# Kernel tuning notes

Hardware: AMD Instinct MI355X
Metric: run time of the kernel (lower is better)

The kernel has to match this reference:

```python
import jax, jax.numpy as jnp
import numpy as np

N = 128   # image_size == proj_size
C = 16    # channels
B = 1
NUM_AP = 1
AP_ANGLES = np.linspace(0.0, 0.0, NUM_AP).tolist()
APLT_ANGLES = np.linspace(0.0, np.pi / 2, 2).tolist()
EPS = 1e-5


def _conv3d(x, w, b):
    # x: [B,C,D,H,W], w: [O,I,3,3,3]
    y = jax.lax.conv_general_dilated(
        x, w, window_strides=(1, 1, 1), padding='SAME',
        dimension_numbers=('NCDHW', 'OIDHW', 'NCDHW'))
    return y + b[None, :, None, None, None]


def _instance_norm(x):
    # InstanceNorm3d, affine=False: normalize per (batch, channel) over D,H,W
    m = x.mean(axis=(2, 3, 4), keepdims=True)
    v = x.var(axis=(2, 3, 4), keepdims=True)
    return (x - m) * jax.lax.rsqrt(v + EPS)


def _resblock(x, w1, b1, w2, b2):
    out = jax.nn.relu(_instance_norm(_conv3d(x, w1, b1)))
    out = _instance_norm(_conv3d(out, w2, b2)) + x
    return jax.nn.relu(out)


def _backproject(proj):
    # proj: [B,C,A,Z,U] -> volume [B,C,Z,N,N] (parallel-beam smear-back)
    c = (N - 1) / 2.0
    ys, xs = jnp.meshgrid(jnp.arange(N, dtype=jnp.float32),
                          jnp.arange(N, dtype=jnp.float32), indexing='ij')
    vol = jnp.zeros((proj.shape[0], proj.shape[1], proj.shape[3], N, N), proj.dtype)
    for a, th in enumerate(AP_ANGLES):
        u = np.cos(th) * (ys - c) + np.sin(th) * (xs - c) + c  # [N,N] detector coord
        u0 = jnp.clip(jnp.floor(u).astype(jnp.int32), 0, N - 2)
        w = u - u0.astype(u.dtype)
        p = proj[:, :, a]                     # [B,C,Z,U]
        g = p[..., u0] * (1.0 - w) + p[..., u0 + 1] * w   # [B,C,Z,N,N]
        valid = (u >= 0.0) & (u <= N - 1.0)
        vol = vol + jnp.where(valid, g, 0.0)
    return vol / float(len(AP_ANGLES))


def _forward_project(vol):
    # vol: [B,C,Z,H,W] -> proj [B,C,A,Z,U] (line integrals per z-slice)
    c = (N - 1) / 2.0
    uu, tt = jnp.meshgrid(jnp.arange(N, dtype=jnp.float32),
                          jnp.arange(N, dtype=jnp.float32), indexing='ij')
    projs = []
    for th in APLT_ANGLES:
        y = c + (uu - c) * np.cos(th) - (tt - c) * np.sin(th)
        x = c + (uu - c) * np.sin(th) + (tt - c) * np.cos(th)
        y0 = jnp.clip(jnp.floor(y).astype(jnp.int32), 0, N - 2)
        x0 = jnp.clip(jnp.floor(x).astype(jnp.int32), 0, N - 2)
        wy = y - y0.astype(y.dtype)
        wx = x - x0.astype(x.dtype)
        g = (vol[:, :, :, y0, x0] * (1 - wy) * (1 - wx)
             + vol[:, :, :, y0 + 1, x0] * wy * (1 - wx)
             + vol[:, :, :, y0, x0 + 1] * (1 - wy) * wx
             + vol[:, :, :, y0 + 1, x0 + 1] * wy * wx)   # [B,C,Z,U,T]
        valid = (y >= 0.0) & (y <= N - 1.0) & (x >= 0.0) & (x <= N - 1.0)
        projs.append(jnp.where(valid, g, 0.0).sum(axis=-1))  # sum over ray param t
    return jnp.stack(projs, axis=2)  # [B,C,A,Z,U]


def setup_inputs() -> dict:
    key = jax.random.key(0)
    ks = jax.random.split(key, 9)
    scale = 1.0 / np.sqrt(C * 27)
    inp = {'projection_data': jax.random.normal(ks[0], (B, C, NUM_AP, N, N), jnp.float32)}
    for i, name in enumerate(['a1', 'a2', 'b1', 'b2']):
        inp['w_' + name] = jax.random.normal(ks[1 + 2 * i], (C, C, 3, 3, 3), jnp.float32) * scale
        inp['b_' + name] = jax.random.normal(ks[2 + 2 * i], (C,), jnp.float32) * 0.01
    return inp


def reference(projection_data, w_a1, b_a1, w_a2, b_a2, w_b1, b_b1, w_b2, b_b2):
    vol = _backproject(projection_data)
    vol = _resblock(vol, w_a1, b_a1, w_a2, b_a2)
    vol = _resblock(vol, w_b1, b_b1, w_b2, b_b2)
    return _forward_project(vol)
```

## Files before the change

### kernel.cpp

```cpp
#include <hip/hip_runtime.h>


typedef unsigned short u16;
typedef unsigned int   u32;
using s16x8 = __attribute__((ext_vector_type(8))) short;
using f32x4 = __attribute__((ext_vector_type(4))) float;

#define IN_ELEMS 262144
#define MN_ELEMS 4194304
#define WS_NEED  28505408ull

__device__ __forceinline__ float bf2f(u16 h) {
    union { u32 u; float f; } v; v.u = ((u32)h) << 16; return v.f;
}
__device__ __forceinline__ u16 f2bf(float f) {
    union { float f; u32 u; } v; v.f = f;
    u32 u = v.u;
    return (u16)((u + 0x7fffu + ((u >> 16) & 1u)) >> 16);
}
__device__ __forceinline__ float ldin(const void* p, int i, int bf) {
    return bf ? bf2f(((const u16*)p)[i]) : ((const float*)p)[i];
}
__device__ __forceinline__ u16 ldbf(const void* p, int i, int bf) {
    return bf ? ((const u16*)p)[i] : f2bf(((const float*)p)[i]);
}
__device__ __forceinline__ void unpack8(uint4 a, float* f) {
    u32 w[4] = {a.x, a.y, a.z, a.w};
#pragma unroll
    for (int i = 0; i < 4; i++) {
        f[2*i]   = bf2f((u16)(w[i] & 0xffff));
        f[2*i+1] = bf2f((u16)(w[i] >> 16));
    }
}
__device__ __forceinline__ void unpack4(uint2 a, float* f) {
    f[0] = bf2f((u16)(a.x & 0xffff)); f[1] = bf2f((u16)(a.x >> 16));
    f[2] = bf2f((u16)(a.y & 0xffff)); f[3] = bf2f((u16)(a.y >> 16));
}

__global__ void sentinel_k(u16* __restrict__ out, int n)
{
    int i = blockIdx.x * 256 + threadIdx.x;
    if (i < n) out[i] = 0x4640;
}

__global__ __launch_bounds__(256) void wprep_prep_k(
    const void* __restrict__ w0, const void* __restrict__ w1,
    const void* __restrict__ w2, const void* __restrict__ w3,
    const void* __restrict__ b0, const void* __restrict__ b1,
    const void* __restrict__ b2, const void* __restrict__ b3,
    const void* __restrict__ proj,
    float* __restrict__ st, int* __restrict__ flag,
    float* __restrict__ biasf, float* __restrict__ w2d,
    float* __restrict__ pz, u16* __restrict__ afrag,
    float* __restrict__ I0, u16* __restrict__ M0)
{
    const int tid = threadIdx.x;
    const u16* pp = (const u16*)w0;
    int cnt = 0;
    for (int i = 0; i < 32; i++) {
        int e = (pp[2 * i] >> 7) & 0xFF;
        if (e >= 64 && e <= 130) cnt++;
    }
    const int bf = (cnt >= 24) ? 1 : 0;
    const void* WS[4] = {w0, w1, w2, w3};
    const void* BS[4] = {b0, b1, b2, b3};
    const int b = blockIdx.x;

    if (b >= 135) {
        const int bb = b - 135;
        const int d = bb >> 2;
        const int ys = (bb & 3) * 32;
        for (int i = tid; i < 512; i += 256) {
            int y = ys + (i >> 4), c = i & 15;
            I0[(d * 128 + y) * 16 + c] = ldin(proj, c * 16384 + d * 128 + y, bf);
        }
        for (int i = tid; i < 1024; i += 256) {
            int y = ys + (i >> 5), x = (i >> 1) & 15, hh = i & 1;
            bool on = (x <= 4) | (x == 7) | (x >= 8 && x < 12);
            u32 pw[4] = {0u, 0u, 0u, 0u};
            if (on) {
#pragma unroll
                for (int j = 0; j < 4; j++) {
                    int c0 = hh * 8 + 2 * j;
                    u16 a = f2bf(ldin(proj, c0 * 16384 + d * 128 + y, bf));
                    u16 bb2 = f2bf(ldin(proj, (c0 + 1) * 16384 + d * 128 + y, bf));
                    pw[j] = (u32)a | ((u32)bb2 << 16);
                }
            }
            *(uint4*)(M0 + ((d * 128 + y) << 8) + (x << 4) + hh * 8) =
                make_uint4(pw[0], pw[1], pw[2], pw[3]);
        }
        return;
    }

    if (b < 18) {
        int gi = b * 256 + tid;
        int L = gi / 1152, r = gi - L * 1152;
        int fi = r >> 6, l = r & 63;
        int kzky = fi >> 1, grp = fi & 1;
        int kz = kzky / 3, ky = kzky % 3;
        int n = l & 15, g = l >> 4, h = g & 1, kxs = g >> 1;
        int kx = grp * 2 + kxs;
        u16 v[8];
#pragma unroll
        for (int e = 0; e < 8; e++) {
            int ci = h * 8 + e;
            v[e] = (kx <= 2) ? ldbf(WS[L], n * 432 + ci * 27 + kz * 9 + ky * 3 + kx, bf)
                             : (u16)0;
        }
#pragma unroll
        for (int e = 0; e < 8; e++) afrag[gi * 8 + e] = v[e];
    } else if (b == 18) {
        st[tid] = 0.f;
        if (tid == 0) *flag = bf;
        if (tid < 64) biasf[tid] = ldin(BS[tid >> 4], tid & 15, bf);
    } else if (b < 99) {
        int i = (b - 19) * 256 + tid;
        pz[i] = 0.f;
    } else {
        int gi = (b - 99) * 256 + tid;
        int L = gi / 2304, r = gi - L * 2304;
        int tap = r >> 8, ci = (r >> 4) & 15, co = r & 15;
        int kz = tap / 3, ky = tap % 3;
        float s = 0.f;
#pragma unroll
        for (int kx = 0; kx < 3; kx++)
            s += ldin(WS[L], (co * 16 + ci) * 27 + kz * 9 + ky * 3 + kx, bf);
        w2d[gi] = s;
    }
}

template <int NORM, int RES, int WXB>
__global__ __launch_bounds__(256) void layer_k(
    const float* __restrict__ Iin, const u16* __restrict__ Min,
    const void* __restrict__ proj, const float* __restrict__ stP,
    const int* __restrict__ flagp,
    const float* __restrict__ w2dL, const u16* __restrict__ afragL,
    const float* __restrict__ biasL,
    float* __restrict__ Iout, u16* __restrict__ Mout,
    float* __restrict__ IXB, u16* __restrict__ MXB,
    float* __restrict__ st_out)
{
    __shared__ __align__(16) char smem_raw[27904];
    const int tid = threadIdx.x;
    const int bf = RES ? *flagp : 0;

    if (blockIdx.x < 256) {
        float* smem = (float*)smem_raw;
        float* wsl  = smem;
        float* pin  = smem + 2304;
        float* sred = smem + 5670;
        float* sA   = smem + 5702;
        const int d  = blockIdx.x >> 1;
        const int y0 = (blockIdx.x & 1) * 64;
        if (tid < 32) {
            sred[tid] = 0.f;
            if (NORM) {
                const float inv = 1.f / 2097152.f;
                int c = tid & 15;
                float m = stP[c] * inv;
                sA[tid] = (tid < 16) ? m : rsqrtf(stP[16 + c] * inv - m * m + 1e-5f);
            }
        }
        for (int i = tid; i < 2304; i += 256) wsl[i] = w2dL[i];
        if (NORM) __syncthreads();
        for (int i = tid; i < 3168; i += 256) {
            int p = i / 1056, r = i - p * 1056;
            int row = r >> 4, c = r & 15;
            int zz = d + p - 1, gy = y0 + row - 1;
            float v = 0.f;
            if ((unsigned)zz < 128u && (unsigned)gy < 128u) {
                v = Iin[(zz * 128 + gy) * 16 + c];
                if (NORM) {
                    float res = RES ? ldin(proj, c * 16384 + zz * 128 + gy, bf) : 0.f;
                    v = fmaxf((v - sA[c]) * sA[16 + c] + res, 0.f);
                }
                if (WXB && p == 1 && row >= 1 && row <= 64)
                    IXB[(d * 128 + gy) * 16 + c] = v;
            }
            pin[p * 1122 + row * 17 + c] = v;
        }
        __syncthreads();

        const int yl = tid & 63, h = tid >> 6;
        float acc[4];
#pragma unroll
        for (int cc = 0; cc < 4; cc++) acc[cc] = biasL[h * 4 + cc];
#pragma unroll
        for (int kz = 0; kz < 3; kz++) {
#pragma unroll
            for (int ky = 0; ky < 3; ky++) {
                const float* rowb = &pin[kz * 1122 + (yl + ky) * 17];
                const float* wrow = &wsl[(kz * 3 + ky) * 256 + h * 4];
#pragma unroll
                for (int ci = 0; ci < 16; ci++) {
                    float v = rowb[ci];
#pragma unroll
                    for (int cc = 0; cc < 4; cc++)
                        acc[cc] = fmaf(v, wrow[ci * 16 + cc], acc[cc]);
                }
            }
        }
        const int e = (d * 128 + y0 + yl) * 16 + h * 4;
        *(float4*)(Iout + e) = make_float4(acc[0], acc[1], acc[2], acc[3]);
        float s[4], q[4];
#pragma unroll
        for (int cc = 0; cc < 4; cc++) { s[cc] = acc[cc]; q[cc] = acc[cc] * acc[cc]; }
#pragma unroll
        for (int off = 1; off < 64; off <<= 1) {
#pragma unroll
            for (int cc = 0; cc < 4; cc++) {
                s[cc] += __shfl_down(s[cc], off, 64);
                q[cc] += __shfl_down(q[cc], off, 64);
            }
        }
        if ((tid & 63) == 0) {
#pragma unroll
            for (int cc = 0; cc < 4; cc++) {
                atomicAdd(&sred[h * 4 + cc], s[cc]);
                atomicAdd(&sred[16 + h * 4 + cc], q[cc]);
            }
        }
        __syncthreads();
        if (tid < 32) atomicAdd(&st_out[tid], 120.f * sred[tid]);
        return;
    }

    u16*   stage = (u16*)smem_raw;
    float* sred  = (float*)(smem_raw + 27648);
    float* sA    = (float*)(smem_raw + 27776);
    const int mb = blockIdx.x - 256;
    const int z  = mb & 127;
    const int yt = mb >> 7;
    const int l = tid & 63, w = tid >> 6;
    const int n = l & 15, g = l >> 4, h = g & 1, kxs = g >> 1;
    const int y0 = yt * 16 + w * 4;
    const int y0b = yt * 16;

    if (tid < 32) {
        sred[tid] = 0.f;
        if (NORM) {
            const float inv = 1.f / 2097152.f;
            int c = tid & 15;
            float m = stP[c] * inv;
            sA[tid] = (tid < 16) ? m : rsqrtf(stP[16 + c] * inv - m * m + 1e-5f);
        }
    }
    if (NORM) __syncthreads();

    for (int i = tid; i < 1728; i += 256) {
        int r = i >> 5, p = i & 31;
        int kz = r / 18, yr = r - kz * 18;
        int gz = z + kz - 1, gy = y0b + yr - 1;
        uint4 v = make_uint4(0u, 0u, 0u, 0u);
        bool inb = ((unsigned)gz < 128u) & ((unsigned)gy < 128u);
        if (!NORM) {
            if (inb) v = *(const uint4*)(Min + (((gz << 7) + gy) << 8) + p * 8);
        } else {
            int x = p >> 1, hh = p & 1;
            bool realc = (x < 4) | (x >= 8 && x < 12);
            bool ghost = (x == 4) | (x == 7);
            if (inb & (realc | ghost)) {
                float f[8];
                if (realc) {
                    uint4 raw = *(const uint4*)(Min + (((gz << 7) + gy) << 8) + p * 8);
                    unpack8(raw, f);
                } else {
                    const float* ip = Iin + ((gz * 128 + gy) * 16 + hh * 8);
                    float4 a  = *(const float4*)(ip);
                    float4 b2 = *(const float4*)(ip + 4);
                    f[0] = a.x;  f[1] = a.y;  f[2] = a.z;  f[3] = a.w;
                    f[4] = b2.x; f[5] = b2.y; f[6] = b2.z; f[7] = b2.w;
                }
                float vals[8];
#pragma unroll
                for (int j = 0; j < 8; j++) {
                    int c = hh * 8 + j;
                    float res = RES ? ldin(proj, c * 16384 + gz * 128 + gy, bf) : 0.f;
                    vals[j] = fmaxf((f[j] - sA[c]) * sA[16 + c] + res, 0.f);
                }
                u32 pw[4];
#pragma unroll
                for (int j = 0; j < 4; j++)
                    pw[j] = (u32)f2bf(vals[2*j]) | ((u32)f2bf(vals[2*j+1]) << 16);
                v = make_uint4(pw[0], pw[1], pw[2], pw[3]);
            }
            if (WXB && kz == 1 && yr >= 1 && yr <= 16)
                *(uint4*)(MXB + (((z << 7) + gy) << 8) + p * 8) = v;
        }
        *(uint4*)(stage + r * 256 + p * 8) = v;
    }

    s16x8 af[18];
#pragma unroll
    for (int fi = 0; fi < 18; fi++)
        af[fi] = *(const s16x8*)(afragL + (fi * 64 + l) * 8);
    f32x4 binit = *(const f32x4*)(biasL + g * 4);
    __syncthreads();

    f32x4 acc[4];
#pragma unroll
    for (int yl = 0; yl < 4; yl++) acc[yl] = binit;

    const int x0c = n + kxs - 1;
    const int x1c = x0c + 2;
    const bool v0ok = (unsigned)x0c < 16u;
    const bool v1ok = (unsigned)x1c < 16u;

#pragma unroll
    for (int kz = 0; kz < 3; kz++) {
#pragma unroll
        for (int yin = 0; yin < 6; yin++) {
            const u16* rowp = stage + (kz * 18 + (w << 2) + yin) * 256 + h * 8;
            uint4 q0 = make_uint4(0u, 0u, 0u, 0u);
            uint4 q1 = make_uint4(0u, 0u, 0u, 0u);
            if (v0ok) q0 = *(const uint4*)(rowp + (x0c << 4));
            if (v1ok) q1 = *(const uint4*)(rowp + (x1c << 4));
            s16x8 f0 = __builtin_bit_cast(s16x8, q0);
            s16x8 f1 = __builtin_bit_cast(s16x8, q1);
#pragma unroll
            for (int ky = 0; ky < 3; ky++) {
                const int yl = yin - ky;
                if (yl >= 0 && yl < 4) {
                    acc[yl] = __builtin_amdgcn_mfma_f32_16x16x32_bf16(af[(kz * 3 + ky) * 2],     f0, acc[yl], 0, 0, 0);
                    acc[yl] = __builtin_amdgcn_mfma_f32_16x16x32_bf16(af[(kz * 3 + ky) * 2 + 1], f1, acc[yl], 0, 0, 0);
                }
            }
        }
    }

    const float inc = (((n >> 2) & 1) == 0) ? 1.f : 0.f;
    float sr[4] = {0.f, 0.f, 0.f, 0.f}, qr[4] = {0.f, 0.f, 0.f, 0.f};
#pragma unroll
    for (int yl = 0; yl < 4; yl++) {
        const int gy = y0 + yl;
        u32 lo = (u32)f2bf(acc[yl][0]) | ((u32)f2bf(acc[yl][1]) << 16);
        u32 hi = (u32)f2bf(acc[yl][2]) | ((u32)f2bf(acc[yl][3]) << 16);
        *(uint2*)(Mout + (((z << 7) + gy) << 8) + (n << 4) + g * 4) = make_uint2(lo, hi);
#pragma unroll
        for (int r = 0; r < 4; r++) {
            sr[r] += inc * acc[yl][r];
            qr[r] = fmaf(inc * acc[yl][r], acc[yl][r], qr[r]);
        }
    }
#pragma unroll
    for (int off = 1; off < 16; off <<= 1) {
#pragma unroll
        for (int r = 0; r < 4; r++) {
            sr[r] += __shfl_down(sr[r], off, 16);
            qr[r] += __shfl_down(qr[r], off, 16);
        }
    }
    __syncthreads();
    if (n == 0) {
#pragma unroll
        for (int r = 0; r < 4; r++) {
            atomicAdd(&sred[g * 4 + r], sr[r]);
            atomicAdd(&sred[16 + g * 4 + r], qr[r]);
        }
    }
    __syncthreads();
    if (tid < 32) atomicAdd(&st_out[tid], sred[tid]);
}

__global__ __launch_bounds__(256) void fproj1_k(
    const float* __restrict__ I4, const float* __restrict__ IXB,
    const u16* __restrict__ M4, const u16* __restrict__ MXB,
    const float* __restrict__ stL, const int* __restrict__ flagp,
    void* __restrict__ out,
    float* __restrict__ P, float* __restrict__ PS, float* __restrict__ P0)
{
    __shared__ float sA[32];
    const int bf = *flagp;
    const int d = blockIdx.x >> 1;
    const int half = blockIdx.x & 1;
    const int tid = threadIdx.x;
    if (tid < 32) {
        const float inv = 1.f / 2097152.f;
        int c = tid & 15;
        float m = stL[c] * inv;
        sA[tid] = (tid < 16) ? m : rsqrtf(stL[16 + c] * inv - m * m + 1e-5f);
    }
    __syncthreads();

    const int yl = tid & 63, y = half * 64 + yl;
    const int h = tid >> 6, c0 = h * 4;

    float v2d[4], row[4];
    {
        const int e = (d * 128 + y) * 16 + c0;
        float4 a = *(const float4*)(I4 + e);
        float4 x = *(const float4*)(IXB + e);
        float ia[4] = {a.x, a.y, a.z, a.w};
        float xa[4] = {x.x, x.y, x.z, x.w};
#pragma unroll
        for (int cc = 0; cc < 4; cc++) {
            int c = c0 + cc;
            v2d[cc] = fmaxf((ia[cc] - sA[c]) * sA[16 + c] + xa[cc], 0.f);
            row[cc] = 120.f * v2d[cc];
        }
    }
    float colp[8][4];
#pragma unroll
    for (int j = 0; j < 8; j++) {
        const int m = (j < 4) ? j : j + 4;
        const int e = ((d * 128 + y) << 8) + (m << 4) + c0;
        float f4[4], fx[4];
        unpack4(*(const uint2*)(M4 + e), f4);
        unpack4(*(const uint2*)(MXB + e), fx);
#pragma unroll
        for (int cc = 0; cc < 4; cc++) {
            int c = c0 + cc;
            float v = fmaxf((f4[cc] - sA[c]) * sA[16 + c] + fx[cc], 0.f);
            row[cc] += v;
            colp[j][cc] = v;
        }
    }
#pragma unroll
    for (int cc = 0; cc < 4; cc++) {
        int oi = ((c0 + cc) * 2) * 16384 + d * 128 + y;
        if (bf) ((u16*)out)[oi] = f2bf(row[cc]); else ((float*)out)[oi] = row[cc];
    }
#pragma unroll
    for (int off = 1; off < 64; off <<= 1) {
#pragma unroll
        for (int cc = 0; cc < 4; cc++) {
            v2d[cc] += __shfl_down(v2d[cc], off, 64);
#pragma unroll
            for (int j = 0; j < 8; j++)
                colp[j][cc] += __shfl_down(colp[j][cc], off, 64);
        }
    }
    if (yl == 0) {
#pragma unroll
        for (int cc = 0; cc < 4; cc++) {
            atomicAdd(&PS[d * 16 + c0 + cc], v2d[cc]);
#pragma unroll
            for (int j = 0; j < 8; j++)
                atomicAdd(&P[(d * 8 + j) * 16 + c0 + cc], colp[j][cc]);
            if (half == 0) P0[d * 16 + c0 + cc] = colp[0][cc];
        }
    }
}

__global__ __launch_bounds__(256) void fproj2_k(
    const float* __restrict__ P, const float* __restrict__ PS,
    const float* __restrict__ P0, const int* __restrict__ flagp,
    void* __restrict__ out)
{
    const int bf = *flagp;
    const int d = blockIdx.x;
    const int tid = threadIdx.x;
    for (int i = tid; i < 2048; i += 256) {
        int c = i >> 7, u = i & 127;
        float v;
        if (u == 0)        v = P0[d * 16 + c];
        else if (u < 4)    v = P[(d * 8 + u) * 16 + c];
        else if (u >= 124) v = P[(d * 8 + (u - 120)) * 16 + c];
        else               v = PS[d * 16 + c];
        int oi = (c * 2 + 1) * 16384 + d * 128 + u;
        if (bf) ((u16*)out)[oi] = f2bf(v); else ((float*)out)[oi] = v;
    }
}

extern "C" void kernel_launch(void* const* d_in, const int* in_sizes, int n_in,
                              void* d_out, int out_size, void* d_ws, size_t ws_size,
                              hipStream_t stream)
{
    if (ws_size < WS_NEED) {
        sentinel_k<<<(out_size + 255) / 256, 256, 0, stream>>>((u16*)d_out, out_size);
        return;
    }
    const void* proj = d_in[0];
    const void* w1 = d_in[1]; const void* b1 = d_in[2];
    const void* w2 = d_in[3]; const void* b2 = d_in[4];
    const void* w3 = d_in[5]; const void* b3 = d_in[6];
    const void* w4 = d_in[7]; const void* b4 = d_in[8];

    float* I_A  = (float*)d_ws;
    float* I_B  = I_A + IN_ELEMS;
    float* I_XB = I_B + IN_ELEMS;
    u16*   M_A  = (u16*)(I_XB + IN_ELEMS);
    u16*   M_B  = M_A + MN_ELEMS;
    u16*   M_XB = M_B + MN_ELEMS;
    float* st    = (float*)(M_XB + MN_ELEMS);
    int*   flag  = (int*)(st + 256);
    float* biasf = (float*)(flag + 16);
    float* w2d   = biasf + 64;
    float* P     = w2d + 9216;
    float* PS    = P + 16384;
    float* P0    = PS + 2048;
    u16*   afrag = (u16*)(P0 + 2048);

    wprep_prep_k<<<647, 256, 0, stream>>>(w1, w2, w3, w4, b1, b2, b3, b4, proj,
                                          st, flag, biasf, w2d, P, afrag, I_A, M_A);

    dim3 lg(1280), cb(256);
    layer_k<0,0,0><<<lg, cb, 0, stream>>>(I_A, M_A, proj, st, flag,
                                          w2d + 0,    afrag + 0,     biasf + 0,
                                          I_B, M_B, nullptr, nullptr, st + 0);
    layer_k<1,0,0><<<lg, cb, 0, stream>>>(I_B, M_B, proj, st + 0, flag,
                                          w2d + 2304, afrag + 9216,  biasf + 16,
                                          I_A, M_A, nullptr, nullptr, st + 64);
    layer_k<1,1,1><<<lg, cb, 0, stream>>>(I_A, M_A, proj, st + 64, flag,
                                          w2d + 4608, afrag + 18432, biasf + 32,
                                          I_B, M_B, I_XB, M_XB, st + 128);
    layer_k<1,0,0><<<lg, cb, 0, stream>>>(I_B, M_B, proj, st + 128, flag,
                                          w2d + 6912, afrag + 27648, biasf + 48,
                                          I_A, M_A, nullptr, nullptr, st + 192);
    fproj1_k<<<256, cb, 0, stream>>>(I_A, I_XB, M_A, M_XB, st + 192, flag, d_out, P, PS, P0);
    fproj2_k<<<128, cb, 0, stream>>>(P, PS, P0, flag, d_out);
}
```

Measured before the change: 211.4 us.

## Split 2D-path conv blocks finer and spread instance-norm stat atomics over banks

The per-z 2D convolution path now uses 1024 blocks, each covering 16 rows, with one thread per output (row, channel) and float4 LDS reads, instead of 256 blocks of 64 rows. Instance-norm statistics are accumulated into 8 separate banks chosen by block index, and a new helper sums the banks when reading them back. This is meant to improve load balance and occupancy for the small 2D path and to cut global atomic contention on the statistics counters. In exchange the workspace grows slightly, each reader does 8x more stat loads, and the halo reload fraction rises with the smaller tiles.

Result: faster. 201.0 us (-5.0%).

```diff
diff --git a/kernel.cpp b/kernel.cpp
--- a/kernel.cpp
+++ b/kernel.cpp
@@ -8,7 +8,7 @@
 
 #define IN_ELEMS 262144
 #define MN_ELEMS 4194304
-#define WS_NEED  28505408ull
+#define WS_NEED  28508480ull
 
 __device__ __forceinline__ float bf2f(u16 h) {
     union { u32 u; float f; } v; v.u = ((u32)h) << 16; return v.f;
@@ -35,6 +35,21 @@
 __device__ __forceinline__ void unpack4(uint2 a, float* f) {
     f[0] = bf2f((u16)(a.x & 0xffff)); f[1] = bf2f((u16)(a.x >> 16));
     f[2] = bf2f((u16)(a.y & 0xffff)); f[3] = bf2f((u16)(a.y >> 16));
+}
+
+__device__ __forceinline__ void stat8(const float* __restrict__ stP, int tid,
+                                      float* __restrict__ sA)
+{
+    const float inv = 1.f / 2097152.f;
+    int c = tid & 15;
+    float ssum = 0.f, qsum = 0.f;
+#pragma unroll
+    for (int b2 = 0; b2 < 8; b2++) {
+        ssum += stP[b2 * 32 + c];
+        qsum += stP[b2 * 32 + 16 + c];
+    }
+    float m = ssum * inv;
+    sA[tid] = (tid < 16) ? m : rsqrtf(qsum * inv - m * m + 1e-5f);
 }
 
 __global__ void sentinel_k(u16* __restrict__ out, int n)
@@ -111,7 +126,7 @@
 #pragma unroll
         for (int e = 0; e < 8; e++) afrag[gi * 8 + e] = v[e];
     } else if (b == 18) {
-        st[tid] = 0.f;
+        for (int i = tid; i < 1024; i += 256) st[i] = 0.f;
         if (tid == 0) *flag = bf;
         if (tid < 64) biasf[tid] = ldin(BS[tid >> 4], tid & 15, bf);
     } else if (b < 99) {
@@ -144,30 +159,27 @@
     __shared__ __align__(16) char smem_raw[27904];
     const int tid = threadIdx.x;
     const int bf = RES ? *flagp : 0;
-
-    if (blockIdx.x < 256) {
+    const int bank = (blockIdx.x & 7) * 32;
+
+    if (blockIdx.x < 1024) {
         float* smem = (float*)smem_raw;
         float* wsl  = smem;
         float* pin  = smem + 2304;
-        float* sred = smem + 5670;
-        float* sA   = smem + 5702;
-        const int d  = blockIdx.x >> 1;
-        const int y0 = (blockIdx.x & 1) * 64;
+        float* sred = smem + 3384;
+        float* sA   = smem + 3416;
+        const int d  = blockIdx.x >> 3;
+        const int yo = (blockIdx.x & 7) * 16;
         if (tid < 32) {
             sred[tid] = 0.f;
-            if (NORM) {
-                const float inv = 1.f / 2097152.f;
-                int c = tid & 15;
-                float m = stP[c] * inv;
-                sA[tid] = (tid < 16) ? m : rsqrtf(stP[16 + c] * inv - m * m + 1e-5f);
-            }
-        }
-        for (int i = tid; i < 2304; i += 256) wsl[i] = w2dL[i];
+            if (NORM) stat8(stP, tid, sA);
+        }
+        for (int i = tid; i < 576; i += 256)
+            *(float4*)(wsl + i * 4) = *(const float4*)(w2dL + i * 4);
         if (NORM) __syncthreads();
-        for (int i = tid; i < 3168; i += 256) {
-            int p = i / 1056, r = i - p * 1056;
+        for (int i = tid; i < 864; i += 256) {
+            int p = i / 288, r = i - p * 288;
             int row = r >> 4, c = r & 15;
-            int zz = d + p - 1, gy = y0 + row - 1;
+            int zz = d + p - 1, gy = yo + row - 1;
             float v = 0.f;
             if ((unsigned)zz < 128u && (unsigned)gy < 128u) {
                 v = Iin[(zz * 128 + gy) * 16 + c];
@@ -175,61 +187,48 @@
                     float res = RES ? ldin(proj, c * 16384 + zz * 128 + gy, bf) : 0.f;
                     v = fmaxf((v - sA[c]) * sA[16 + c] + res, 0.f);
                 }
-                if (WXB && p == 1 && row >= 1 && row <= 64)
+                if (WXB && p == 1 && row >= 1 && row <= 16)
                     IXB[(d * 128 + gy) * 16 + c] = v;
             }
-            pin[p * 1122 + row * 17 + c] = v;
+            pin[p * 360 + row * 20 + c] = v;
         }
         __syncthreads();
 
-        const int yl = tid & 63, h = tid >> 6;
-        float acc[4];
-#pragma unroll
-        for (int cc = 0; cc < 4; cc++) acc[cc] = biasL[h * 4 + cc];
+        const int c = tid & 15, yl = tid >> 4;
+        float acc = biasL[c];
 #pragma unroll
         for (int kz = 0; kz < 3; kz++) {
 #pragma unroll
             for (int ky = 0; ky < 3; ky++) {
-                const float* rowb = &pin[kz * 1122 + (yl + ky) * 17];
-                const float* wrow = &wsl[(kz * 3 + ky) * 256 + h * 4];
-#pragma unroll
-                for (int ci = 0; ci < 16; ci++) {
-                    float v = rowb[ci];
-#pragma unroll
-                    for (int cc = 0; cc < 4; cc++)
-                        acc[cc] = fmaf(v, wrow[ci * 16 + cc], acc[cc]);
+                const float4* rowb = (const float4*)(pin + kz * 360 + (yl + ky) * 20);
+                const float* wrow = wsl + (kz * 3 + ky) * 256 + c;
+#pragma unroll
+                for (int qd = 0; qd < 4; qd++) {
+                    float4 vq = rowb[qd];
+                    acc = fmaf(vq.x, wrow[(qd * 4 + 0) * 16], acc);
+                    acc = fmaf(vq.y, wrow[(qd * 4 + 1) * 16], acc);
+                    acc = fmaf(vq.z, wrow[(qd * 4 + 2) * 16], acc);
+                    acc = fmaf(vq.w, wrow[(qd * 4 + 3) * 16], acc);
                 }
             }
         }
-        const int e = (d * 128 + y0 + yl) * 16 + h * 4;
-        *(float4*)(Iout + e) = make_float4(acc[0], acc[1], acc[2], acc[3]);
-        float s[4], q[4];
-#pragma unroll
-        for (int cc = 0; cc < 4; cc++) { s[cc] = acc[cc]; q[cc] = acc[cc] * acc[cc]; }
-#pragma unroll
-        for (int off = 1; off < 64; off <<= 1) {
-#pragma unroll
-            for (int cc = 0; cc < 4; cc++) {
-                s[cc] += __shfl_down(s[cc], off, 64);
-                q[cc] += __shfl_down(q[cc], off, 64);
-            }
-        }
-        if ((tid & 63) == 0) {
-#pragma unroll
-            for (int cc = 0; cc < 4; cc++) {
-                atomicAdd(&sred[h * 4 + cc], s[cc]);
-                atomicAdd(&sred[16 + h * 4 + cc], q[cc]);
-            }
+        Iout[(d * 128 + yo + yl) * 16 + c] = acc;
+        float s = acc, q = acc * acc;
+        s += __shfl_xor(s, 16, 64); s += __shfl_xor(s, 32, 64);
+        q += __shfl_xor(q, 16, 64); q += __shfl_xor(q, 32, 64);
+        if ((tid & 63) < 16) {
+            atomicAdd(&sred[c], s);
+            atomicAdd(&sred[16 + c], q);
         }
         __syncthreads();
-        if (tid < 32) atomicAdd(&st_out[tid], 120.f * sred[tid]);
+        if (tid < 32) atomicAdd(&st_out[bank + tid], 120.f * sred[tid]);
         return;
     }
 
     u16*   stage = (u16*)smem_raw;
     float* sred  = (float*)(smem_raw + 27648);
     float* sA    = (float*)(smem_raw + 27776);
-    const int mb = blockIdx.x - 256;
+    const int mb = blockIdx.x - 1024;
     const int z  = mb & 127;
     const int yt = mb >> 7;
     const int l = tid & 63, w = tid >> 6;
@@ -239,12 +238,7 @@
 
     if (tid < 32) {
         sred[tid] = 0.f;
-        if (NORM) {
-            const float inv = 1.f / 2097152.f;
-            int c = tid & 15;
-            float m = stP[c] * inv;
-            sA[tid] = (tid < 16) ? m : rsqrtf(stP[16 + c] * inv - m * m + 1e-5f);
-        }
+        if (NORM) stat8(stP, tid, sA);
     }
     if (NORM) __syncthreads();
 
@@ -360,7 +354,7 @@
         }
     }
     __syncthreads();
-    if (tid < 32) atomicAdd(&st_out[tid], sred[tid]);
+    if (tid < 32) atomicAdd(&st_out[bank + tid], sred[tid]);
 }
 
 __global__ __launch_bounds__(256) void fproj1_k(
@@ -375,12 +369,7 @@
     const int d = blockIdx.x >> 1;
     const int half = blockIdx.x & 1;
     const int tid = threadIdx.x;
-    if (tid < 32) {
-        const float inv = 1.f / 2097152.f;
-        int c = tid & 15;
-        float m = stL[c] * inv;
-        sA[tid] = (tid < 16) ? m : rsqrtf(stL[16 + c] * inv - m * m + 1e-5f);
-    }
+    if (tid < 32) stat8(stL, tid, sA);
     __syncthreads();
 
     const int yl = tid & 63, y = half * 64 + yl;
@@ -484,7 +473,7 @@
     u16*   M_B  = M_A + MN_ELEMS;
     u16*   M_XB = M_B + MN_ELEMS;
     float* st    = (float*)(M_XB + MN_ELEMS);
-    int*   flag  = (int*)(st + 256);
+    int*   flag  = (int*)(st + 1024);
     float* biasf = (float*)(flag + 16);
     float* w2d   = biasf + 64;
     float* P     = w2d + 9216;
@@ -495,19 +484,19 @@
     wprep_prep_k<<<647, 256, 0, stream>>>(w1, w2, w3, w4, b1, b2, b3, b4, proj,
                                           st, flag, biasf, w2d, P, afrag, I_A, M_A);
 
-    dim3 lg(1280), cb(256);
+    dim3 lg(2048), cb(256);
     layer_k<0,0,0><<<lg, cb, 0, stream>>>(I_A, M_A, proj, st, flag,
                                           w2d + 0,    afrag + 0,     biasf + 0,
                                           I_B, M_B, nullptr, nullptr, st + 0);
     layer_k<1,0,0><<<lg, cb, 0, stream>>>(I_B, M_B, proj, st + 0, flag,
                                           w2d + 2304, afrag + 9216,  biasf + 16,
-                                          I_A, M_A, nullptr, nullptr, st + 64);
-    layer_k<1,1,1><<<lg, cb, 0, stream>>>(I_A, M_A, proj, st + 64, flag,
+                                          I_A, M_A, nullptr, nullptr, st + 256);
+    layer_k<1,1,1><<<lg, cb, 0, stream>>>(I_A, M_A, proj, st + 256, flag,
                                           w2d + 4608, afrag + 18432, biasf + 32,
-                                          I_B, M_B, I_XB, M_XB, st + 128);
-    layer_k<1,0,0><<<lg, cb, 0, stream>>>(I_B, M_B, proj, st + 128, flag,
+                                          I_B, M_B, I_XB, M_XB, st + 512);
+    layer_k<1,0,0><<<lg, cb, 0, stream>>>(I_B, M_B, proj, st + 512, flag,
                                           w2d + 6912, afrag + 27648, biasf + 48,
-                                          I_A, M_A, nullptr, nullptr, st + 192);
-    fproj1_k<<<256, cb, 0, stream>>>(I_A, I_XB, M_A, M_XB, st + 192, flag, d_out, P, PS, P0);
+                                          I_A, M_A, nullptr, nullptr, st + 768);
+    fproj1_k<<<256, cb, 0, stream>>>(I_A, I_XB, M_A, M_XB, st + 768, flag, d_out, P, PS, P0);
     fproj2_k<<<128, cb, 0, stream>>>(P, PS, P0, flag, d_out);
 }
```
